# Kernel tuning notes

Measured on AMD Instinct MI355X. Metric: run time of the kernel, lower is better.

The kernel has to match this reference:

```python
import jax, jax.numpy as jnp
import numpy as np

B, H, W, C = 8, 64, 64, 256  # N = H*W = 4096, pooled length N//2 = 2048


def setup_inputs() -> dict:
    key = jax.random.key(0)
    k1, k2, k3, k4 = jax.random.split(key, 4)
    scale = np.sqrt(2.0 / C).astype(np.float32)  # he_normal for 1x1 conv
    return {
        "x": jax.random.normal(k1, (B, H, W, C), dtype=jnp.float32),
        "w_theta": jax.random.normal(k2, (C, C), dtype=jnp.float32) * scale,
        "w_phi": jax.random.normal(k3, (C, C), dtype=jnp.float32) * scale,
        "w_g": jax.random.normal(k4, (C, C), dtype=jnp.float32) * scale,
    }


def _maxpool1d(z):
    # MaxPool1D(pool_size=2, strides=2, padding='valid') over axis 1
    b, n, c = z.shape
    return jnp.max(z.reshape(b, n // 2, 2, c), axis=2)


def reference(x, w_theta, w_phi, w_g):
    b, h, w, c = x.shape
    n = h * w
    xf = x.reshape(b, n, c)                       # [B, N, C]
    theta = xf @ w_theta                          # [B, N, C] (1x1 conv)
    phi = _maxpool1d(xf @ w_phi)                  # [B, N//2, C]
    f = jnp.einsum('bnc,bmc->bnm', theta, phi)    # [B, N, N//2] affinity
    f = jax.nn.softmax(f, axis=-1)
    g = _maxpool1d(xf @ w_g)                      # [B, N//2, C]
    y = jnp.einsum('bnm,bmc->bnc', f, g)          # [B, N, C]
    y = y.reshape(b, h, w, c)
    return x + y                                  # residual
```

## Files before the change

### kernel.cpp

```cpp
#include <hip/hip_runtime.h>
#include <stdint.h>

#define CC 256
#define NN 4096
#define MM 2048
#define BB 8
#define NROWS (BB*NN)
#define PROWS (BB*MM)

typedef __attribute__((ext_vector_type(8))) short    short8;
typedef __attribute__((ext_vector_type(8))) _Float16 half8;
typedef __attribute__((ext_vector_type(4))) float    float4v;

__device__ __forceinline__ unsigned short f2bf(float f) {
    unsigned int u = __float_as_uint(f);
    u += 0x7fffu + ((u >> 16) & 1u);
    return (unsigned short)(u >> 16);
}
__device__ __forceinline__ float bf2f(unsigned short h) {
    return __uint_as_float(((unsigned int)h) << 16);
}
__device__ __forceinline__ unsigned short f2h(float f) {
    union { _Float16 h; unsigned short u; } cv; cv.h = (_Float16)f; return cv.u;
}
__device__ __forceinline__ float h2f(unsigned short u) {
    union { _Float16 h; unsigned short u; } cv; cv.u = u; return (float)cv.h;
}

__global__ __launch_bounds__(256) void xsplit_kernel(
    const float* __restrict__ x,
    unsigned short* __restrict__ x_hi,
    unsigned short* __restrict__ x_lo)
{
    const size_t i = ((size_t)blockIdx.x*256 + threadIdx.x) * 8;
    float4v a0 = *(const float4v*)(x + i);
    float4v a1 = *(const float4v*)(x + i + 4);
    short8 h, l;
    #pragma unroll
    for (int j = 0; j < 4; ++j) {
        unsigned short h0 = f2bf(a0[j]);
        h[j]   = (short)h0; l[j]   = (short)f2bf(a0[j] - bf2f(h0));
        unsigned short h1 = f2bf(a1[j]);
        h[4+j] = (short)h1; l[4+j] = (short)f2bf(a1[j] - bf2f(h1));
    }
    *(short8*)(x_hi + i) = h;
    *(short8*)(x_lo + i) = l;
}

__global__ void wsplit_kernel(const float* __restrict__ w_theta,
                              const float* __restrict__ w_phi,
                              const float* __restrict__ w_g,
                              unsigned short* __restrict__ wT_hi,
                              unsigned short* __restrict__ wT_lo)
{
    __shared__ float tile[64][65];
    const int widx = blockIdx.z;
    const int kt = blockIdx.x, ct = blockIdx.y;
    const float* w = (widx == 0) ? w_theta : (widx == 1) ? w_phi : w_g;
    const int t  = threadIdx.x;
    const int tc = t & 63, tr = t >> 6;
    #pragma unroll
    for (int i = 0; i < 16; ++i) {
        const int lk = tr*16 + i;
        tile[lk][tc] = w[(size_t)(kt*64 + lk)*CC + ct*64 + tc];
    }
    __syncthreads();
    #pragma unroll
    for (int i = 0; i < 16; ++i) {
        const int lc = tr*16 + i;
        float v = tile[tc][lc];
        const int c = ct*64 + lc, k = kt*64 + tc;
        unsigned short hh = f2bf(v);
        size_t o = ((size_t)widx*CC + c)*CC + k;
        wT_hi[o] = hh;
        wT_lo[o] = f2bf(v - bf2f(hh));
    }
}

__global__ __launch_bounds__(256, 4) void proj_kernel(
    const unsigned short* __restrict__ x_hi,
    const unsigned short* __restrict__ x_lo,
    const unsigned short* __restrict__ wT_hi,
    const unsigned short* __restrict__ wT_lo,
    unsigned short* __restrict__ th,
    unsigned short* __restrict__ ph,
    unsigned short* __restrict__ g_t)
{
    __shared__ unsigned short wt_hi[64*136];
    __shared__ unsigned short wt_lo[64*136];

    const int tid  = threadIdx.x;
    const int rb   = blockIdx.x & 511;
    const int cv   = blockIdx.x >> 9;
    const int r0   = rb * 64;
    const int widx = cv >> 2;
    const int wc0  = (cv & 3) * 64;
    const unsigned short* wThp = wT_hi + ((size_t)widx*CC + wc0)*CC;
    const unsigned short* wTlp = wT_lo + ((size_t)widx*CC + wc0)*CC;
    const bool split3 = (widx < 2);

    const int wv   = tid >> 6;
    const int lane = tid & 63;
    const int quad = lane >> 4;
    const int l15  = lane & 15;
    const int arow = r0 + wv*16 + l15;
    const unsigned short* axh = x_hi + (size_t)arow*CC + quad*8;
    const unsigned short* axl = x_lo + (size_t)arow*CC + quad*8;

    float4v acc[4];
    #pragma unroll
    for (int nf = 0; nf < 4; ++nf) acc[nf] = (float4v){0.f,0.f,0.f,0.f};

    for (int h = 0; h < 2; ++h) {
        __syncthreads();
        {
            const int j    = tid & 63;
            const int kseg = tid >> 6;
            const size_t base = (size_t)j*CC + h*128 + kseg*32;
            const unsigned short* sh = wThp + base;
            unsigned short* dh = &wt_hi[j*136 + kseg*32];
            #pragma unroll
            for (int u = 0; u < 4; ++u)
                *(uint4*)(dh + u*8) = *(const uint4*)(sh + u*8);
            if (split3) {
                const unsigned short* sl = wTlp + base;
                unsigned short* dl = &wt_lo[j*136 + kseg*32];
                #pragma unroll
                for (int u = 0; u < 4; ++u)
                    *(uint4*)(dl + u*8) = *(const uint4*)(sl + u*8);
            }
        }
        __syncthreads();

        #pragma unroll
        for (int ks = 0; ks < 4; ++ks) {
            short8 a_hi = *(const short8*)(axh + h*128 + ks*32);
            short8 a_lo;
            if (split3) a_lo = *(const short8*)(axl + h*128 + ks*32);
            #pragma unroll
            for (int nf = 0; nf < 4; ++nf) {
                const int wrow = nf*16 + l15;
                short8 b_hi = *(const short8*)&wt_hi[wrow*136 + ks*32 + quad*8];
                acc[nf] = __builtin_amdgcn_mfma_f32_16x16x32_bf16(a_hi, b_hi, acc[nf], 0,0,0);
                if (split3) {
                    short8 b_lo = *(const short8*)&wt_lo[wrow*136 + ks*32 + quad*8];
                    acc[nf] = __builtin_amdgcn_mfma_f32_16x16x32_bf16(a_hi, b_lo, acc[nf], 0,0,0);
                    acc[nf] = __builtin_amdgcn_mfma_f32_16x16x32_bf16(a_lo, b_hi, acc[nf], 0,0,0);
                }
            }
        }
    }

    const int rowbase = r0 + wv*16 + quad*4;
    if (widx == 0) {
        #pragma unroll
        for (int nf = 0; nf < 4; ++nf) {
            const int c = wc0 + nf*16 + l15;
            #pragma unroll
            for (int r = 0; r < 4; ++r)
                th[(size_t)(rowbase + r)*CC + c] = f2h(acc[nf][r]);
        }
    } else if (widx == 1) {
        #pragma unroll
        for (int nf = 0; nf < 4; ++nf) {
            const int c = wc0 + nf*16 + l15;
            #pragma unroll
            for (int rp = 0; rp < 2; ++rp) {
                float v = fmaxf(acc[nf][2*rp], acc[nf][2*rp+1]);
                const int prow = rowbase/2 + rp;
                ph[(size_t)prow*CC + c] = f2h(v);
            }
        }
    } else {
        #pragma unroll
        for (int nf = 0; nf < 4; ++nf) {
            const int c = wc0 + nf*16 + l15;
            #pragma unroll
            for (int rp = 0; rp < 2; ++rp) {
                float v = fmaxf(acc[nf][2*rp], acc[nf][2*rp+1]);
                const int prow = rowbase/2 + rp;
                const int b = prow >> 11;
                const int m = prow & 2047;
                g_t[((size_t)b*CC + c)*MM + m] = f2bf(v);
            }
        }
    }
}

__global__ void phimean_kernel(const unsigned short* __restrict__ ph,
                               float* __restrict__ phbar)
{
    const int b = blockIdx.x >> 6, chunk = blockIdx.x & 63;
    const int c = threadIdx.x;
    const size_t base = ((size_t)b*MM + chunk*32)*CC + c;
    float s = 0.f;
    for (int r = 0; r < 32; ++r) s += h2f(ph[base + (size_t)r*CC]);
    atomicAdd(&phbar[b*CC + c], s * (1.0f/MM));
}

__global__ __launch_bounds__(256, 3) void attn_kernel(
    const float* __restrict__ x,
    const unsigned short* __restrict__ th,
    const unsigned short* __restrict__ ph,
    const unsigned short* __restrict__ g_t,
    const float* __restrict__ phbar,
    float* __restrict__ out)
{
    __shared__ unsigned short s_ph[2][32*264];
    __shared__ unsigned short s_p[4][16*40];
    __shared__ float          s_l[64];

    const int tid  = threadIdx.x;
    const int q0   = blockIdx.x * 64;
    const int b    = q0 >> 12;
    const int wv   = tid >> 6;
    const int lane = tid & 63;
    const int quad = lane >> 4;
    const int l15  = lane & 15;

    const int sti = tid >> 3;
    const int stc = (tid & 7) * 32;
    const size_t phbase = (size_t)b * MM * CC;
    const unsigned short* stsrc = ph + phbase + (size_t)sti*CC + stc;

    half8 t_hi[8];
    {
        const unsigned short* bh = th + (size_t)(q0 + wv*16 + l15)*CC;
        #pragma unroll
        for (int ks = 0; ks < 8; ++ks)
            t_hi[ks] = *(const half8*)(bh + ks*32 + quad*8);
    }

    float sh128[4];
    {
        float sp = 0.f;
        #pragma unroll
        for (int ks = 0; ks < 8; ++ks) {
            const int k0 = ks*32 + quad*8;
            float4v m0 = *(const float4v*)&phbar[b*CC + k0];
            float4v m1 = *(const float4v*)&phbar[b*CC + k0 + 4];
            #pragma unroll
            for (int j = 0; j < 4; ++j) {
                sp += (float)t_hi[ks][j]   * m0[j];
                sp += (float)t_hi[ks][4+j] * m1[j];
            }
        }
        sp += __shfl_xor(sp, 16);
        sp += __shfl_xor(sp, 32);
        #pragma unroll
        for (int r = 0; r < 4; ++r)
            sh128[r] = __shfl(sp, quad*4 + r) + 128.f;
    }

    float4v O[4][4];
    #pragma unroll
    for (int rt = 0; rt < 4; ++rt)
        #pragma unroll
        for (int ct = 0; ct < 4; ++ct) O[rt][ct] = (float4v){0.f,0.f,0.f,0.f};
    float4v accl = (float4v){0.f,0.f,0.f,0.f};

    short8 ones;
    #pragma unroll
    for (int j = 0; j < 8; ++j) ones[j] = (short)0x3F80;

    const unsigned short* gl =
        g_t + ((size_t)b*CC + wv*64 + l15)*MM + quad*8;

    {
        unsigned short* dh = &s_ph[0][sti*264 + stc];
        #pragma unroll
        for (int u = 0; u < 4; ++u)
            *(uint4*)(dh + u*8) = *(const uint4*)(stsrc + u*8);
    }
    __syncthreads();

    for (int kt = 0; kt < 64; ++kt) {
        const int key0 = kt * 32;
        const int cur  = kt & 1;

        uint4 stg[4];
        if (kt < 63) {
            const unsigned short* sn = stsrc + (size_t)(key0 + 32)*CC;
            #pragma unroll
            for (int u = 0; u < 4; ++u) stg[u] = *(const uint4*)(sn + u*8);
        }
        short8 gf[4];
        #pragma unroll
        for (int ct = 0; ct < 4; ++ct)
            gf[ct] = *(const short8*)(gl + (size_t)ct*16*MM + key0);

        float4v S0 = (float4v){0.f,0.f,0.f,0.f};
        float4v S1 = (float4v){0.f,0.f,0.f,0.f};
        #pragma unroll
        for (int ks = 0; ks < 8; ++ks) {
            half8 b0 = *(const half8*)&s_ph[cur][( 0 + l15)*264 + ks*32 + quad*8];
            half8 b1 = *(const half8*)&s_ph[cur][(16 + l15)*264 + ks*32 + quad*8];
            S0 = __builtin_amdgcn_mfma_f32_16x16x32_f16(t_hi[ks], b0, S0, 0,0,0);
            S1 = __builtin_amdgcn_mfma_f32_16x16x32_f16(t_hi[ks], b1, S1, 0,0,0);
        }

        unsigned short* pw = &s_p[wv][0];
        #pragma unroll
        for (int r = 0; r < 4; ++r) {
            float a0 = fminf(fmaxf(S0[r] - sh128[r], -85.f), 85.f);
            float a1 = fminf(fmaxf(S1[r] - sh128[r], -85.f), 85.f);
            pw[(quad*4 + r)*40 + l15]      = f2bf(__expf(a0));
            pw[(quad*4 + r)*40 + 16 + l15] = f2bf(__expf(a1));
        }
        asm volatile("s_waitcnt lgkmcnt(0)" ::: "memory");
        short8 pown = *(const short8*)&s_p[wv][l15*40 + quad*8];
        accl = __builtin_amdgcn_mfma_f32_16x16x32_bf16(pown, ones, accl, 0,0,0);

        if (kt < 63) {
            unsigned short* dh = &s_ph[cur ^ 1][sti*264 + stc];
            #pragma unroll
            for (int u = 0; u < 4; ++u) *(uint4*)(dh + u*8) = stg[u];
        }
        __syncthreads();

        #pragma unroll
        for (int rt = 0; rt < 4; ++rt) {
            short8 pA = *(const short8*)&s_p[rt][l15*40 + quad*8];
            #pragma unroll
            for (int ct = 0; ct < 4; ++ct)
                O[rt][ct] = __builtin_amdgcn_mfma_f32_16x16x32_bf16(pA, gf[ct], O[rt][ct], 0,0,0);
        }
        __syncthreads();
    }

    if (l15 == 0) {
        #pragma unroll
        for (int r = 0; r < 4; ++r) s_l[wv*16 + quad*4 + r] = accl[r];
    }
    __syncthreads();

    #pragma unroll
    for (int rt = 0; rt < 4; ++rt) {
        #pragma unroll
        for (int r = 0; r < 4; ++r) {
            const int row = q0 + rt*16 + quad*4 + r;
            const float rl = 1.0f / s_l[rt*16 + quad*4 + r];
            #pragma unroll
            for (int ct = 0; ct < 4; ++ct) {
                const int c = wv*64 + ct*16 + l15;
                const size_t idx = (size_t)row*CC + c;
                out[idx] = x[idx] + O[rt][ct][r] * rl;
            }
        }
    }
}

extern "C" void kernel_launch(void* const* d_in, const int* in_sizes, int n_in,
                              void* d_out, int out_size, void* d_ws, size_t ws_size,
                              hipStream_t stream) {
    const float* x       = (const float*)d_in[0];
    const float* w_theta = (const float*)d_in[1];
    const float* w_phi   = (const float*)d_in[2];
    const float* w_g     = (const float*)d_in[3];
    float* out = (float*)d_out;

    unsigned short* th    = (unsigned short*)d_ws;
    unsigned short* ph    = th    + (size_t)NROWS*CC;
    unsigned short* g_t   = ph    + (size_t)PROWS*CC;
    unsigned short* x_hi  = g_t   + (size_t)PROWS*CC;
    unsigned short* x_lo  = x_hi  + (size_t)NROWS*CC;
    unsigned short* wT_hi = x_lo  + (size_t)NROWS*CC;
    unsigned short* wT_lo = wT_hi + (size_t)3*CC*CC;
    float*          phbar = (float*)(wT_lo + (size_t)3*CC*CC);

    hipMemsetAsync(phbar, 0, BB*CC*sizeof(float), stream);
    xsplit_kernel<<<NROWS*CC/8/256, 256, 0, stream>>>(x, x_hi, x_lo);
    wsplit_kernel<<<dim3(4,4,3), 256, 0, stream>>>(w_theta, w_phi, w_g, wT_hi, wT_lo);
    proj_kernel<<<6144, 256, 0, stream>>>(x_hi, x_lo, wT_hi, wT_lo, th, ph, g_t);
    phimean_kernel<<<512, 256, 0, stream>>>(ph, phbar);
    attn_kernel<<<NROWS/64, 256, 0, stream>>>(x, th, ph, g_t, phbar, out);
}
```

Measured before the change: 285.1 us.

## Software-pipeline attention PV MFMA with double-buffered P and reuse weights in projection

The attention loop now double-buffers the probability tile so each iteration's P·G MFMAs consume the previous tile while the next QK scores are computed. This removes one of the two block barriers per key tile, and the final tile is drained after the loop. The projection kernel loads its full 64x256 weight slice into shared memory once and loops over four row blocks, cutting repeated weight staging and the launch count. Blocks in the attention grid are interleaved across batches, and the launch bounds drop to 2 waves, which lowers occupancy in exchange for more registers.

```diff
diff --git a/kernel.cpp b/kernel.cpp
--- a/kernel.cpp
+++ b/kernel.cpp
@@ -77,7 +77,7 @@
     }
 }
 
-__global__ __launch_bounds__(256, 4) void proj_kernel(
+__global__ __launch_bounds__(256, 2) void proj_kernel(
     const unsigned short* __restrict__ x_hi,
     const unsigned short* __restrict__ x_lo,
     const unsigned short* __restrict__ wT_hi,
@@ -86,102 +86,100 @@
     unsigned short* __restrict__ ph,
     unsigned short* __restrict__ g_t)
 {
-    __shared__ unsigned short wt_hi[64*136];
-    __shared__ unsigned short wt_lo[64*136];
+    __shared__ unsigned short wt_hi[64*264];
+    __shared__ unsigned short wt_lo[64*264];
 
     const int tid  = threadIdx.x;
-    const int rb   = blockIdx.x & 511;
-    const int cv   = blockIdx.x >> 9;
-    const int r0   = rb * 64;
+    const int rg   = blockIdx.x & 127;
+    const int cv   = blockIdx.x >> 7;
     const int widx = cv >> 2;
     const int wc0  = (cv & 3) * 64;
-    const unsigned short* wThp = wT_hi + ((size_t)widx*CC + wc0)*CC;
-    const unsigned short* wTlp = wT_lo + ((size_t)widx*CC + wc0)*CC;
     const bool split3 = (widx < 2);
+
+    {
+        const int j    = tid & 63;
+        const int kseg = tid >> 6;
+        const size_t gbase = ((size_t)widx*CC + wc0 + j)*CC + kseg*64;
+        const unsigned short* sh = wT_hi + gbase;
+        unsigned short* dh = &wt_hi[j*264 + kseg*64];
+        #pragma unroll
+        for (int u = 0; u < 8; ++u)
+            *(uint4*)(dh + u*8) = *(const uint4*)(sh + u*8);
+        if (split3) {
+            const unsigned short* sl = wT_lo + gbase;
+            unsigned short* dl = &wt_lo[j*264 + kseg*64];
+            #pragma unroll
+            for (int u = 0; u < 8; ++u)
+                *(uint4*)(dl + u*8) = *(const uint4*)(sl + u*8);
+        }
+    }
+    __syncthreads();
 
     const int wv   = tid >> 6;
     const int lane = tid & 63;
     const int quad = lane >> 4;
     const int l15  = lane & 15;
-    const int arow = r0 + wv*16 + l15;
-    const unsigned short* axh = x_hi + (size_t)arow*CC + quad*8;
-    const unsigned short* axl = x_lo + (size_t)arow*CC + quad*8;
-
-    float4v acc[4];
-    #pragma unroll
-    for (int nf = 0; nf < 4; ++nf) acc[nf] = (float4v){0.f,0.f,0.f,0.f};
-
-    for (int h = 0; h < 2; ++h) {
-        __syncthreads();
-        {
-            const int j    = tid & 63;
-            const int kseg = tid >> 6;
-            const size_t base = (size_t)j*CC + h*128 + kseg*32;
-            const unsigned short* sh = wThp + base;
-            unsigned short* dh = &wt_hi[j*136 + kseg*32];
-            #pragma unroll
-            for (int u = 0; u < 4; ++u)
-                *(uint4*)(dh + u*8) = *(const uint4*)(sh + u*8);
-            if (split3) {
-                const unsigned short* sl = wTlp + base;
-                unsigned short* dl = &wt_lo[j*136 + kseg*32];
-                #pragma unroll
-                for (int u = 0; u < 4; ++u)
-                    *(uint4*)(dl + u*8) = *(const uint4*)(sl + u*8);
-            }
-        }
-        __syncthreads();
-
-        #pragma unroll
-        for (int ks = 0; ks < 4; ++ks) {
-            short8 a_hi = *(const short8*)(axh + h*128 + ks*32);
+
+    for (int irb = 0; irb < 4; ++irb) {
+        const int r0   = (rg*4 + irb) * 64;
+        const int arow = r0 + wv*16 + l15;
+        const unsigned short* axh = x_hi + (size_t)arow*CC + quad*8;
+        const unsigned short* axl = x_lo + (size_t)arow*CC + quad*8;
+
+        float4v acc[4];
+        #pragma unroll
+        for (int nf = 0; nf < 4; ++nf) acc[nf] = (float4v){0.f,0.f,0.f,0.f};
+
+        #pragma unroll
+        for (int ksf = 0; ksf < 8; ++ksf) {
+            short8 a_hi = *(const short8*)(axh + ksf*32);
             short8 a_lo;
-            if (split3) a_lo = *(const short8*)(axl + h*128 + ks*32);
+            if (split3) a_lo = *(const short8*)(axl + ksf*32);
             #pragma unroll
             for (int nf = 0; nf < 4; ++nf) {
                 const int wrow = nf*16 + l15;
-                short8 b_hi = *(const short8*)&wt_hi[wrow*136 + ks*32 + quad*8];
+                short8 b_hi = *(const short8*)&wt_hi[wrow*264 + ksf*32 + quad*8];
                 acc[nf] = __builtin_amdgcn_mfma_f32_16x16x32_bf16(a_hi, b_hi, acc[nf], 0,0,0);
                 if (split3) {
-                    short8 b_lo = *(const short8*)&wt_lo[wrow*136 + ks*32 + quad*8];
+                    short8 b_lo = *(const short8*)&wt_lo[wrow*264 + ksf*32 + quad*8];
                     acc[nf] = __builtin_amdgcn_mfma_f32_16x16x32_bf16(a_hi, b_lo, acc[nf], 0,0,0);
                     acc[nf] = __builtin_amdgcn_mfma_f32_16x16x32_bf16(a_lo, b_hi, acc[nf], 0,0,0);
                 }
             }
         }
-    }
-
-    const int rowbase = r0 + wv*16 + quad*4;
-    if (widx == 0) {
-        #pragma unroll
-        for (int nf = 0; nf < 4; ++nf) {
-            const int c = wc0 + nf*16 + l15;
-            #pragma unroll
-            for (int r = 0; r < 4; ++r)
-                th[(size_t)(rowbase + r)*CC + c] = f2h(acc[nf][r]);
-        }
-    } else if (widx == 1) {
-        #pragma unroll
-        for (int nf = 0; nf < 4; ++nf) {
-            const int c = wc0 + nf*16 + l15;
-            #pragma unroll
-            for (int rp = 0; rp < 2; ++rp) {
-                float v = fmaxf(acc[nf][2*rp], acc[nf][2*rp+1]);
-                const int prow = rowbase/2 + rp;
-                ph[(size_t)prow*CC + c] = f2h(v);
-            }
-        }
-    } else {
-        #pragma unroll
-        for (int nf = 0; nf < 4; ++nf) {
-            const int c = wc0 + nf*16 + l15;
-            #pragma unroll
-            for (int rp = 0; rp < 2; ++rp) {
-                float v = fmaxf(acc[nf][2*rp], acc[nf][2*rp+1]);
-                const int prow = rowbase/2 + rp;
-                const int b = prow >> 11;
-                const int m = prow & 2047;
-                g_t[((size_t)b*CC + c)*MM + m] = f2bf(v);
+
+        const int rowbase = r0 + wv*16 + quad*4;
+        if (widx == 0) {
+            #pragma unroll
+            for (int nf = 0; nf < 4; ++nf) {
+                const int c = wc0 + nf*16 + l15;
+                #pragma unroll
+                for (int r = 0; r < 4; ++r)
+                    th[(size_t)(rowbase + r)*CC + c] = f2h(acc[nf][r]);
+            }
+        } else if (widx == 1) {
+            #pragma unroll
+            for (int nf = 0; nf < 4; ++nf) {
+                const int c = wc0 + nf*16 + l15;
+                #pragma unroll
+                for (int rp = 0; rp < 2; ++rp) {
+                    float v = fmaxf(acc[nf][2*rp], acc[nf][2*rp+1]);
+                    const int prow = rowbase/2 + rp;
+                    ph[(size_t)prow*CC + c] = f2h(v);
+                }
+            }
+        } else {
+            #pragma unroll
+            for (int nf = 0; nf < 4; ++nf) {
+                const int c = wc0 + nf*16 + l15;
+                #pragma unroll
+                for (int rp = 0; rp < 2; ++rp) {
+                    float v = fmaxf(acc[nf][2*rp], acc[nf][2*rp+1]);
+                    const int prow = rowbase/2 + rp;
+                    const int bb = prow >> 11;
+                    const int m  = prow & 2047;
+                    g_t[((size_t)bb*CC + c)*MM + m] = f2bf(v);
+                }
             }
         }
     }
@@ -198,7 +196,7 @@
     atomicAdd(&phbar[b*CC + c], s * (1.0f/MM));
 }
 
-__global__ __launch_bounds__(256, 3) void attn_kernel(
+__global__ __launch_bounds__(256, 2) void attn_kernel(
     const float* __restrict__ x,
     const unsigned short* __restrict__ th,
     const unsigned short* __restrict__ ph,
@@ -207,12 +205,12 @@
     float* __restrict__ out)
 {
     __shared__ unsigned short s_ph[2][32*264];
-    __shared__ unsigned short s_p[4][16*40];
+    __shared__ unsigned short s_p[2][4][16*40];
     __shared__ float          s_l[64];
 
     const int tid  = threadIdx.x;
-    const int q0   = blockIdx.x * 64;
-    const int b    = q0 >> 12;
+    const int b    = blockIdx.x & 7;
+    const int q0   = b*NN + (blockIdx.x >> 3)*64;
     const int wv   = tid >> 6;
     const int lane = tid & 63;
     const int quad = lane >> 4;
@@ -272,22 +270,23 @@
         for (int u = 0; u < 4; ++u)
             *(uint4*)(dh + u*8) = *(const uint4*)(stsrc + u*8);
     }
-    __syncthreads();
 
     for (int kt = 0; kt < 64; ++kt) {
-        const int key0 = kt * 32;
-        const int cur  = kt & 1;
+        const int cur = kt & 1;
+        __syncthreads();
 
         uint4 stg[4];
         if (kt < 63) {
-            const unsigned short* sn = stsrc + (size_t)(key0 + 32)*CC;
+            const unsigned short* sn = stsrc + (size_t)(kt + 1)*32*CC;
             #pragma unroll
             for (int u = 0; u < 4; ++u) stg[u] = *(const uint4*)(sn + u*8);
         }
         short8 gf[4];
-        #pragma unroll
-        for (int ct = 0; ct < 4; ++ct)
-            gf[ct] = *(const short8*)(gl + (size_t)ct*16*MM + key0);
+        if (kt > 0) {
+            #pragma unroll
+            for (int ct = 0; ct < 4; ++ct)
+                gf[ct] = *(const short8*)(gl + (size_t)ct*16*MM + (kt-1)*32);
+        }
 
         float4v S0 = (float4v){0.f,0.f,0.f,0.f};
         float4v S1 = (float4v){0.f,0.f,0.f,0.f};
@@ -299,7 +298,17 @@
             S1 = __builtin_amdgcn_mfma_f32_16x16x32_f16(t_hi[ks], b1, S1, 0,0,0);
         }
 
-        unsigned short* pw = &s_p[wv][0];
+        if (kt > 0) {
+            #pragma unroll
+            for (int rt = 0; rt < 4; ++rt) {
+                short8 pA = *(const short8*)&s_p[cur^1][rt][l15*40 + quad*8];
+                #pragma unroll
+                for (int ct = 0; ct < 4; ++ct)
+                    O[rt][ct] = __builtin_amdgcn_mfma_f32_16x16x32_bf16(pA, gf[ct], O[rt][ct], 0,0,0);
+            }
+        }
+
+        unsigned short* pw = &s_p[cur][wv][0];
         #pragma unroll
         for (int r = 0; r < 4; ++r) {
             float a0 = fminf(fmaxf(S0[r] - sh128[r], -85.f), 85.f);
@@ -308,7 +317,7 @@
             pw[(quad*4 + r)*40 + 16 + l15] = f2bf(__expf(a1));
         }
         asm volatile("s_waitcnt lgkmcnt(0)" ::: "memory");
-        short8 pown = *(const short8*)&s_p[wv][l15*40 + quad*8];
+        short8 pown = *(const short8*)&s_p[cur][wv][l15*40 + quad*8];
         accl = __builtin_amdgcn_mfma_f32_16x16x32_bf16(pown, ones, accl, 0,0,0);
 
         if (kt < 63) {
@@ -316,16 +325,21 @@
             #pragma unroll
             for (int u = 0; u < 4; ++u) *(uint4*)(dh + u*8) = stg[u];
         }
-        __syncthreads();
-
+    }
+
+    __syncthreads();
+    {
+        short8 gf[4];
+        #pragma unroll
+        for (int ct = 0; ct < 4; ++ct)
+            gf[ct] = *(const short8*)(gl + (size_t)ct*16*MM + 63*32);
         #pragma unroll
         for (int rt = 0; rt < 4; ++rt) {
-            short8 pA = *(const short8*)&s_p[rt][l15*40 + quad*8];
+            short8 pA = *(const short8*)&s_p[1][rt][l15*40 + quad*8];
             #pragma unroll
             for (int ct = 0; ct < 4; ++ct)
                 O[rt][ct] = __builtin_amdgcn_mfma_f32_16x16x32_bf16(pA, gf[ct], O[rt][ct], 0,0,0);
         }
-        __syncthreads();
     }
 
     if (l15 == 0) {
@@ -371,7 +385,7 @@
     hipMemsetAsync(phbar, 0, BB*CC*sizeof(float), stream);
     xsplit_kernel<<<NROWS*CC/8/256, 256, 0, stream>>>(x, x_hi, x_lo);
     wsplit_kernel<<<dim3(4,4,3), 256, 0, stream>>>(w_theta, w_phi, w_g, wT_hi, wT_lo);
-    proj_kernel<<<6144, 256, 0, stream>>>(x_hi, x_lo, wT_hi, wT_lo, th, ph, g_t);
+    proj_kernel<<<1536, 256, 0, stream>>>(x_hi, x_lo, wT_hi, wT_lo, th, ph, g_t);
     phimean_kernel<<<512, 256, 0, stream>>>(ph, phbar);
     attn_kernel<<<NROWS/64, 256, 0, stream>>>(x, th, ph, g_t, phbar, out);
 }
```

Result: slower. 365.9 us (+28.3%).
